# Performance work log

Measured on AMD Instinct MI355X. Metric: run time of the kernel, lower is better.

Reference implementation:

```python
import jax, jax.numpy as jnp
import numpy as np

B, S, DIM, N_CONCEPTS, N_LAYERS = 4, 2048, 1024, 2048, 2


def _phase_linear(x, W, b):
    # x: [b,s,d_in,2]; same real linear applied to real and imag components
    return jnp.einsum('bsdp,od->bsop', x, W) + b[:, None]


def _phase_layernorm(x, gamma, beta, eps=1e-5):
    # per-component LayerNorm over the feature dim with shared affine params
    mu = x.mean(axis=-2, keepdims=True)
    var = x.var(axis=-2, keepdims=True)
    return (x - mu) / jnp.sqrt(var + eps) * gamma[:, None] + beta[:, None]


def setup_inputs() -> dict:
    key = jax.random.key(0)
    ks = jax.random.split(key, 8)
    x = jax.random.normal(ks[0], (B, S, DIM, 2), dtype=jnp.float32)
    concept_memory = jax.random.normal(ks[1], (N_CONCEPTS, DIM, 2), dtype=jnp.float32) * 0.02
    scale = 1.0 / np.sqrt(DIM)
    W_layers = jax.random.normal(ks[2], (N_LAYERS, DIM, DIM), dtype=jnp.float32) * scale
    b_layers = jnp.zeros((N_LAYERS, DIM), dtype=jnp.float32)
    gamma = jnp.ones((N_LAYERS, DIM), dtype=jnp.float32)
    beta = jnp.zeros((N_LAYERS, DIM), dtype=jnp.float32)
    W_out = jax.random.normal(ks[3], (DIM, DIM), dtype=jnp.float32) * scale
    b_out = jnp.zeros((DIM,), dtype=jnp.float32)
    g_out = jnp.ones((DIM,), dtype=jnp.float32)
    beta_out = jnp.zeros((DIM,), dtype=jnp.float32)
    return {"x": x, "concept_memory": concept_memory, "W_layers": W_layers,
            "b_layers": b_layers, "gamma": gamma, "beta": beta,
            "W_out": W_out, "b_out": b_out, "g_out": g_out, "beta_out": beta_out}


def reference(x, concept_memory, W_layers, b_layers, gamma, beta, W_out, b_out, g_out, beta_out):
    xr, xi = x[..., 0], x[..., 1]                       # [b,s,d]
    cr, ci = concept_memory[..., 0], concept_memory[..., 1]  # [n,d]
    # phase-coherence concept attention
    dot_real = jnp.einsum('bsd,nd->bsn', xr, cr) + jnp.einsum('bsd,nd->bsn', xi, ci)
    x_mag = jnp.sqrt((xr ** 2 + xi ** 2).sum(axis=-1, keepdims=True) + 1e-8)   # [b,s,1]
    c_mag = jnp.sqrt((cr ** 2 + ci ** 2).sum(axis=-1) + 1e-8)                  # [n]
    coherence = dot_real / (x_mag * c_mag[None, None, :] + 1e-8)
    concept_attn = jax.nn.softmax(coherence * 2.0, axis=-1)
    concept_retrieved = jnp.einsum('bsn,ndp->bsdp', concept_attn, concept_memory)
    h = x + concept_retrieved * 0.1
    # gated FFN blocks (eval mode: dropout off)
    for l in range(N_LAYERS):
        residual = h
        h = _phase_layernorm(h, gamma[l], beta[l])
        h = _phase_linear(h, W_layers[l], b_layers[l])
        h = jax.nn.gelu(h[..., 0:1], approximate=False) * h
        h = residual + h * 0.1
    out = _phase_layernorm(h, g_out, beta_out)
    out = _phase_linear(out, W_out, b_out)
    return out
```

## Files before the change

kernel.cpp:

```cpp
#include <hip/hip_runtime.h>
#include <hip/hip_bf16.h>

#define ROWS 8192
#define K2   2048
#define NCPT 2048
#define DIMD 1024

using short8 = __attribute__((ext_vector_type(8))) short;
using f32x4  = __attribute__((ext_vector_type(4))) float;

__device__ __forceinline__ unsigned short f2b(float f) {
  __hip_bfloat16 h = __float2bfloat16(f);
  return *reinterpret_cast<unsigned short*>(&h);
}
__device__ __forceinline__ float b2f(unsigned short u) {
  unsigned int x = ((unsigned int)u) << 16;
  return __uint_as_float(x);
}

__device__ __forceinline__ void store_bf16x8(unsigned short* dst, const float4& a, const float4& b) {
  union { unsigned short u[8]; uint4 q; } p;
  p.u[0]=f2b(a.x); p.u[1]=f2b(a.y); p.u[2]=f2b(a.z); p.u[3]=f2b(a.w);
  p.u[4]=f2b(b.x); p.u[5]=f2b(b.y); p.u[6]=f2b(b.z); p.u[7]=f2b(b.w);
  *reinterpret_cast<uint4*>(dst) = p.q;
}
__device__ __forceinline__ void store_bf16x4(unsigned short* dst, float a, float b, float c, float d) {
  union { unsigned short u[4]; uint2 q; } p;
  p.u[0]=f2b(a); p.u[1]=f2b(b); p.u[2]=f2b(c); p.u[3]=f2b(d);
  *reinterpret_cast<uint2*>(dst) = p.q;
}

__device__ __forceinline__ void async_lds16(const void* g, void* l) {
  __builtin_amdgcn_global_load_lds((__attribute__((address_space(1))) void*)g,
                                   (__attribute__((address_space(3))) void*)l, 16, 0, 0);
}

__global__ void cast_row_mag(const float* __restrict__ src, unsigned short* __restrict__ dst,
                             float* __restrict__ mag, int ncol) {
  __shared__ float sred[4];
  int row = blockIdx.x, t = threadIdx.x;
  const float* s = src + (size_t)row * ncol;
  unsigned short* d = dst + (size_t)row * ncol;
  float ss = 0.f;
  for (int i = t * 8; i < ncol; i += 2048) {
    float4 a = *(const float4*)(s + i);
    float4 b = *(const float4*)(s + i + 4);
    ss += a.x*a.x + a.y*a.y + a.z*a.z + a.w*a.w;
    ss += b.x*b.x + b.y*b.y + b.z*b.z + b.w*b.w;
    store_bf16x8(d + i, a, b);
  }
  int lane = t & 63, w = t >> 6;
  for (int o = 32; o; o >>= 1) ss += __shfl_down(ss, o);
  if (lane == 0) sred[w] = ss;
  __syncthreads();
  if (t == 0) mag[row] = sqrtf(sred[0] + sred[1] + sred[2] + sred[3] + 1e-8f);
}

__global__ void cast_f2b(const float* __restrict__ src, unsigned short* __restrict__ dst, int n) {
  int stride = gridDim.x * blockDim.x * 8;
  for (int i = (blockIdx.x * blockDim.x + threadIdx.x) * 8; i < n; i += stride) {
    float4 a = *(const float4*)(src + i);
    float4 b = *(const float4*)(src + i + 4);
    store_bf16x8(dst + i, a, b);
  }
}

__global__ void transpose_f2b(const float* __restrict__ src, unsigned short* __restrict__ dst, int n) {
  __shared__ float tile[32][33];
  int bx = blockIdx.x * 32;
  int by = blockIdx.y * 32;
  int tx = threadIdx.x & 31, ty = threadIdx.x >> 5;
  #pragma unroll
  for (int i = ty; i < 32; i += 8)
    tile[i][tx] = src[(size_t)(by + i) * n + bx + tx];
  __syncthreads();
  #pragma unroll
  for (int i = ty; i < 32; i += 8)
    dst[(size_t)(bx + i) * n + by + tx] = f2b(tile[tx][i]);
}

__global__ void softmax_attn(const unsigned short* __restrict__ logit, unsigned short* __restrict__ attn) {
  __shared__ float sred[4];
  int row = blockIdx.x, t = threadIdx.x;
  int lane = t & 63, w = t >> 6;
  const unsigned short* lr = logit + (size_t)row * NCPT + t * 8;
  short8 lv = *reinterpret_cast<const short8*>(lr);
  float l[8];
  #pragma unroll
  for (int i = 0; i < 8; ++i) l[i] = b2f((unsigned short)lv[i]);
  float m = l[0];
  #pragma unroll
  for (int i = 1; i < 8; ++i) m = fmaxf(m, l[i]);
  for (int o = 32; o; o >>= 1) m = fmaxf(m, __shfl_down(m, o));
  if (lane == 0) sred[w] = m;
  __syncthreads();
  m = fmaxf(fmaxf(sred[0], sred[1]), fmaxf(sred[2], sred[3]));
  __syncthreads();
  float e[8], s = 0.f;
  #pragma unroll
  for (int i = 0; i < 8; ++i) { e[i] = expf(l[i] - m); s += e[i]; }
  for (int o = 32; o; o >>= 1) s += __shfl_down(s, o);
  if (lane == 0) sred[w] = s;
  __syncthreads();
  s = sred[0] + sred[1] + sred[2] + sred[3];
  float inv = 1.f / s;
  float4 A = make_float4(e[0]*inv, e[1]*inv, e[2]*inv, e[3]*inv);
  float4 B = make_float4(e[4]*inv, e[5]*inv, e[6]*inv, e[7]*inv);
  store_bf16x8(attn + (size_t)row * NCPT + t * 8, A, B);
}

__global__ void phase_ln(const float* __restrict__ h, const float* __restrict__ gamma,
                         const float* __restrict__ beta, unsigned short* __restrict__ out) {
  __shared__ float4 s4[4];
  int bs = blockIdx.x, t = threadIdx.x;
  const float* hr = h + (size_t)bs * 2048;
  float4 v0 = *(const float4*)(hr + t * 8);
  float4 v1 = *(const float4*)(hr + t * 8 + 4);
  float r0 = v0.x, i0 = v0.y, r1 = v0.z, i1 = v0.w;
  float r2 = v1.x, i2 = v1.y, r3 = v1.z, i3 = v1.w;
  float4 s;
  s.x = r0 + r1 + r2 + r3;
  s.y = r0*r0 + r1*r1 + r2*r2 + r3*r3;
  s.z = i0 + i1 + i2 + i3;
  s.w = i0*i0 + i1*i1 + i2*i2 + i3*i3;
  int lane = t & 63, w = t >> 6;
  for (int o = 32; o; o >>= 1) {
    s.x += __shfl_down(s.x, o); s.y += __shfl_down(s.y, o);
    s.z += __shfl_down(s.z, o); s.w += __shfl_down(s.w, o);
  }
  if (lane == 0) s4[w] = s;
  __syncthreads();
  float4 T = s4[0];
  #pragma unroll
  for (int i = 1; i < 4; ++i) { T.x += s4[i].x; T.y += s4[i].y; T.z += s4[i].z; T.w += s4[i].w; }
  const float invd = 1.f / 1024.f;
  float mu_r = T.x * invd, var_r = T.y * invd - mu_r * mu_r;
  float mu_i = T.z * invd, var_i = T.w * invd - mu_i * mu_i;
  float is_r = 1.f / sqrtf(var_r + 1e-5f);
  float is_i = 1.f / sqrtf(var_i + 1e-5f);
  float4 g = *(const float4*)(gamma + t * 4);
  float4 b = *(const float4*)(beta + t * 4);
  unsigned short* o0 = out + (size_t)(2 * bs) * 1024 + t * 4;
  unsigned short* o1 = out + (size_t)(2 * bs + 1) * 1024 + t * 4;
  store_bf16x4(o0, (r0-mu_r)*is_r*g.x + b.x, (r1-mu_r)*is_r*g.y + b.y,
                   (r2-mu_r)*is_r*g.z + b.z, (r3-mu_r)*is_r*g.w + b.w);
  store_bf16x4(o1, (i0-mu_i)*is_i*g.x + b.x, (i1-mu_i)*is_i*g.y + b.y,
                   (i2-mu_i)*is_i*g.z + b.z, (i3-mu_i)*is_i*g.w + b.w);
}

template <int EPI>
__global__ __launch_bounds__(512, 2) void gemm256(
    const unsigned short* __restrict__ A, const unsigned short* __restrict__ B,
    int M, int N, int K, void* __restrict__ Cv, const float* __restrict__ aux,
    const float* __restrict__ aux2) {
  __shared__ char lds[131072];
  const int t = threadIdx.x;
  const int l = t & 63;
  const int wid = t >> 6;
  const int wm = wid >> 2, wn = wid & 3;
  const int row0 = blockIdx.y * 256, col0 = blockIdx.x * 256;
  const int NT = K >> 6;

  const int l15 = l & 15, l7 = l & 7, lk = l >> 4;

  f32x4 acc[8][4] = {};
  short8 af[4][2], bf[4][2];

  auto stage = [&](const unsigned short* gmat, int tileRow, int kcol, char* region) {
    const int rsub = t >> 3;
    const int csw = ((t & 7) ^ (rsub & 7)) << 3;
    const unsigned short* g0 = gmat + (size_t)(tileRow + rsub) * K + kcol + csw;
    async_lds16(g0, region + (t & ~63) * 16);
    async_lds16(g0 + (size_t)64 * K, region + 8192 + (t & ~63) * 16);
  };

  stage(A, row0,       0, lds + 0);
  stage(A, row0 + 128, 0, lds + 16384);
  stage(B, col0,       0, lds + 32768);
  stage(B, col0 + 128, 0, lds + 49152);
  if (NT > 1) {
    stage(A, row0, 64, lds + 65536 + 0);
    stage(B, col0, 64, lds + 65536 + 32768);
    asm volatile("s_waitcnt vmcnt(4)" ::: "memory");
  } else {
    asm volatile("s_waitcnt vmcnt(0)" ::: "memory");
  }
  __builtin_amdgcn_s_barrier();
  asm volatile("" ::: "memory");

  for (int tk = 0; tk < NT; ++tk) {
    char* bufC = lds + (tk & 1) * 65536;
    char* bufN = lds + ((tk & 1) ^ 1) * 65536;

    #pragma unroll
    for (int m = 0; m < 4; ++m)
      #pragma unroll
      for (int kh = 0; kh < 2; ++kh) {
        const int r = wm * 64 + m * 16 + l15;
        const int sp = ((((kh << 2) | lk) ^ l7) << 4);
        af[m][kh] = *reinterpret_cast<const short8*>(bufC + r * 128 + sp);
      }
    #pragma unroll
    for (int n = 0; n < 2; ++n)
      #pragma unroll
      for (int kh = 0; kh < 2; ++kh) {
        const int r = wn * 32 + n * 16 + l15;
        const int sp = ((((kh << 2) | lk) ^ l7) << 4);
        bf[n][kh] = *reinterpret_cast<const short8*>(bufC + 32768 + r * 128 + sp);
      }
    if (tk + 1 < NT) stage(A, row0 + 128, (tk + 1) * 64, bufN + 16384);
    asm volatile("" ::: "memory");
    __builtin_amdgcn_s_barrier();
    asm volatile("" ::: "memory");
    __builtin_amdgcn_s_setprio(1);
    #pragma unroll
    for (int kh = 0; kh < 2; ++kh)
      #pragma unroll
      for (int m = 0; m < 4; ++m)
        #pragma unroll
        for (int n = 0; n < 2; ++n)
          acc[m][n] = __builtin_amdgcn_mfma_f32_16x16x32_bf16(af[m][kh], bf[n][kh], acc[m][n], 0, 0, 0);
    __builtin_amdgcn_s_setprio(0);
    asm volatile("" ::: "memory");
    __builtin_amdgcn_s_barrier();
    asm volatile("" ::: "memory");

    #pragma unroll
    for (int n = 2; n < 4; ++n)
      #pragma unroll
      for (int kh = 0; kh < 2; ++kh) {
        const int r = wn * 32 + (n & 1) * 16 + l15;
        const int sp = ((((kh << 2) | lk) ^ l7) << 4);
        bf[n][kh] = *reinterpret_cast<const short8*>(bufC + 49152 + r * 128 + sp);
      }
    if (tk + 1 < NT) stage(B, col0 + 128, (tk + 1) * 64, bufN + 49152);
    asm volatile("" ::: "memory");
    __builtin_amdgcn_s_barrier();
    asm volatile("" ::: "memory");
    __builtin_amdgcn_s_setprio(1);
    #pragma unroll
    for (int kh = 0; kh < 2; ++kh)
      #pragma unroll
      for (int m = 0; m < 4; ++m)
        #pragma unroll
        for (int n = 2; n < 4; ++n)
          acc[m][n] = __builtin_amdgcn_mfma_f32_16x16x32_bf16(af[m][kh], bf[n][kh], acc[m][n], 0, 0, 0);
    __builtin_amdgcn_s_setprio(0);
    asm volatile("" ::: "memory");
    __builtin_amdgcn_s_barrier();
    asm volatile("" ::: "memory");

    #pragma unroll
    for (int m = 0; m < 4; ++m)
      #pragma unroll
      for (int kh = 0; kh < 2; ++kh) {
        const int r = wm * 64 + m * 16 + l15;
        const int sp = ((((kh << 2) | lk) ^ l7) << 4);
        af[m][kh] = *reinterpret_cast<const short8*>(bufC + 16384 + r * 128 + sp);
      }
    if (tk + 2 < NT) stage(A, row0, (tk + 2) * 64, bufC + 0);
    asm volatile("" ::: "memory");
    __builtin_amdgcn_s_barrier();
    asm volatile("" ::: "memory");
    __builtin_amdgcn_s_setprio(1);
    #pragma unroll
    for (int kh = 0; kh < 2; ++kh)
      #pragma unroll
      for (int m = 0; m < 4; ++m)
        #pragma unroll
        for (int n = 0; n < 2; ++n)
          acc[m + 4][n] = __builtin_amdgcn_mfma_f32_16x16x32_bf16(af[m][kh], bf[n][kh], acc[m + 4][n], 0, 0, 0);
    __builtin_amdgcn_s_setprio(0);
    asm volatile("" ::: "memory");
    __builtin_amdgcn_s_barrier();
    asm volatile("" ::: "memory");

    if (tk + 2 < NT) {
      stage(B, col0, (tk + 2) * 64, bufC + 32768);
      asm volatile("s_waitcnt vmcnt(4)" ::: "memory");
    } else {
      asm volatile("s_waitcnt vmcnt(0)" ::: "memory");
    }
    __builtin_amdgcn_s_barrier();
    asm volatile("" ::: "memory");
    __builtin_amdgcn_s_setprio(1);
    #pragma unroll
    for (int kh = 0; kh < 2; ++kh)
      #pragma unroll
      for (int m = 0; m < 4; ++m)
        #pragma unroll
        for (int n = 2; n < 4; ++n)
          acc[m + 4][n] = __builtin_amdgcn_mfma_f32_16x16x32_bf16(af[m][kh], bf[n][kh], acc[m + 4][n], 0, 0, 0);
    __builtin_amdgcn_s_setprio(0);
    asm volatile("" ::: "memory");
    __builtin_amdgcn_s_barrier();
    asm volatile("" ::: "memory");
  }
  asm volatile("s_waitcnt vmcnt(0)" ::: "memory");

  const int cr = lk * 4;
  #pragma unroll
  for (int m = 0; m < 8; ++m) {
    const int gr = row0 + ((m >> 2) << 7) + wm * 64 + ((m & 3) << 4) + cr;
    #pragma unroll
    for (int n = 0; n < 4; ++n) {
      const int gc = col0 + ((n >> 1) << 7) + wn * 32 + ((n & 1) << 4) + l15;
      if constexpr (EPI == 0) {
        unsigned short* C = (unsigned short*)Cv;
        const float cm_ = aux2[gc];
        #pragma unroll
        for (int j = 0; j < 4; ++j) {
          const int r = gr + j;
          float v = 2.f * acc[m][n][j] / (aux[r] * cm_ + 1e-8f);
          C[(size_t)r * N + gc] = f2b(v);
        }
      } else if constexpr (EPI == 1) {
        float* C = (float*)Cv;
        #pragma unroll
        for (int j = 0; j < 4; ++j) {
          const int r = gr + j;
          C[(size_t)r * N + gc] = aux[(size_t)r * N + gc] + 0.1f * acc[m][n][j];
        }
      } else if constexpr (EPI == 2) {
        float* C = (float*)Cv;
        const float bb = aux[gc];
        #pragma unroll
        for (int jj = 0; jj < 2; ++jj) {
          const int r = gr + jj * 2;
          float re = acc[m][n][jj * 2] + bb;
          float im = acc[m][n][jj * 2 + 1] + bb;
          float g = 0.5f * re * (1.f + erff(re * 0.70710678118654752440f));
          size_t idx = (size_t)(r >> 1) * 2048 + (size_t)gc * 2;
          float2 hv = *(float2*)(C + idx);
          hv.x += 0.1f * g * re;
          hv.y += 0.1f * g * im;
          *(float2*)(C + idx) = hv;
        }
      } else {
        float* C = (float*)Cv;
        #pragma unroll
        for (int j = 0; j < 4; ++j) {
          const int r = gr + j;
          C[(size_t)(r >> 1) * 2048 + (size_t)gc * 2 + (r & 1)] = acc[m][n][j] + aux[gc];
        }
      }
    }
  }
}

extern "C" void kernel_launch(void* const* d_in, const int* in_sizes, int n_in,
                              void* d_out, int out_size, void* d_ws, size_t ws_size,
                              hipStream_t stream) {
  const float* x     = (const float*)d_in[0];
  const float* cm    = (const float*)d_in[1];
  const float* Wl    = (const float*)d_in[2];
  const float* bl    = (const float*)d_in[3];
  const float* gamma = (const float*)d_in[4];
  const float* beta  = (const float*)d_in[5];
  const float* Wo    = (const float*)d_in[6];
  const float* bo    = (const float*)d_in[7];
  const float* go    = (const float*)d_in[8];
  const float* bto   = (const float*)d_in[9];
  float* out = (float*)d_out;

  char* p = (char*)d_ws;
  unsigned short* x_bf = (unsigned short*)p; p += (size_t)ROWS * K2 * 2;
  unsigned short* c_bf = (unsigned short*)p; p += (size_t)NCPT * K2 * 2;
  unsigned short* c_T  = (unsigned short*)p; p += (size_t)K2 * NCPT * 2;
  unsigned short* w_bf = (unsigned short*)p; p += (size_t)3 * 1024 * 1024 * 2;
  float* x_mag = (float*)p; p += (size_t)ROWS * 4;
  float* c_mag = (float*)p; p += (size_t)NCPT * 4;
  unsigned short* dot_bf = (unsigned short*)p; p += (size_t)ROWS * NCPT * 2;
  unsigned short* attn   = (unsigned short*)p; p += (size_t)ROWS * NCPT * 2;
  float* h = (float*)p; p += (size_t)ROWS * K2 * 4;
  unsigned short* ln_bf = attn;

  cast_row_mag<<<ROWS, 256, 0, stream>>>(x, x_bf, x_mag, K2);
  cast_row_mag<<<NCPT, 256, 0, stream>>>(cm, c_bf, c_mag, K2);
  transpose_f2b<<<dim3(64, 64), 256, 0, stream>>>(cm, c_T, 2048);
  cast_f2b<<<1024, 256, 0, stream>>>(Wl, w_bf, 2 * 1024 * 1024);
  cast_f2b<<<512, 256, 0, stream>>>(Wo, w_bf + 2 * 1024 * 1024, 1024 * 1024);

  gemm256<0><<<dim3(NCPT / 256, ROWS / 256), 512, 0, stream>>>(
      x_bf, c_bf, ROWS, NCPT, K2, dot_bf, x_mag, c_mag);
  softmax_attn<<<ROWS, 256, 0, stream>>>(dot_bf, attn);
  gemm256<1><<<dim3(K2 / 256, ROWS / 256), 512, 0, stream>>>(
      attn, c_T, ROWS, K2, NCPT, h, x, nullptr);

  for (int l = 0; l < 2; ++l) {
    phase_ln<<<ROWS, 256, 0, stream>>>(h, gamma + l * 1024, beta + l * 1024, ln_bf);
    gemm256<2><<<dim3(DIMD / 256, 2 * ROWS / 256), 512, 0, stream>>>(
        ln_bf, w_bf + (size_t)l * 1024 * 1024, 2 * ROWS, DIMD, DIMD, h, bl + l * 1024, nullptr);
  }

  phase_ln<<<ROWS, 256, 0, stream>>>(h, go, bto, ln_bf);
  gemm256<3><<<dim3(DIMD / 256, 2 * ROWS / 256), 512, 0, stream>>>(
      ln_bf, w_bf + 2 * 1024 * 1024, 2 * ROWS, DIMD, DIMD, out, bo, nullptr);
}
```

Measured before the change: 408.8 us.

## Restructure GEMM prefetch schedule, remap workgroups across XCDs, read residual from bf16

The GEMM pipeline now fully prefetches tile k+1 in the prologue and issues all four quarter-tile loads for k+2 into the current buffer during the loop, waiting on vmcnt(8) and an extra lgkmcnt wait. Workgroup IDs are remapped in chunks of eight so neighbouring tiles land on the same XCD, which should improve L2 reuse. The residual in the attention-output epilogue is read from the bf16 copy of x instead of fp32 x, halving that read traffic but rounding the residual to bf16, which loses precision. A dead readA helper is added. The remap assumes the workgroup count divides by eight, and the prefetch timing changes could introduce races if the waits are wrong.

```diff
diff --git a/kernel.cpp b/kernel.cpp
--- a/kernel.cpp
+++ b/kernel.cpp
@@ -152,15 +152,21 @@
 __global__ __launch_bounds__(512, 2) void gemm256(
     const unsigned short* __restrict__ A, const unsigned short* __restrict__ B,
     int M, int N, int K, void* __restrict__ Cv, const float* __restrict__ aux,
-    const float* __restrict__ aux2) {
+    const float* __restrict__ aux2, const unsigned short* __restrict__ auxb) {
   __shared__ char lds[131072];
   const int t = threadIdx.x;
   const int l = t & 63;
   const int wid = t >> 6;
   const int wm = wid >> 2, wn = wid & 3;
-  const int row0 = blockIdx.y * 256, col0 = blockIdx.x * 256;
+
+  const int nwg = gridDim.x * gridDim.y;
+  int bid = blockIdx.y * gridDim.x + blockIdx.x;
+  const int chunk = nwg >> 3;
+  bid = (bid & 7) * chunk + (bid >> 3);
+  const int row0 = (bid / gridDim.x) * 256;
+  const int col0 = (bid % gridDim.x) * 256;
+
   const int NT = K >> 6;
-
   const int l15 = l & 15, l7 = l & 7, lk = l >> 4;
 
   f32x4 acc[8][4] = {};
@@ -174,14 +180,23 @@
     async_lds16(g0 + (size_t)64 * K, region + 8192 + (t & ~63) * 16);
   };
 
+  auto readA = [&](char* base, int m, int kh) -> short8 {
+    const int r = wm * 64 + m * 16 + l15;
+    const int sp = ((((kh << 1) | (lk >> 1)) * 2 + (lk & 1)) ^ l7) << 4;
+    return *reinterpret_cast<const short8*>(base + r * 128 + sp);
+  };
+  (void)readA;
+
   stage(A, row0,       0, lds + 0);
   stage(A, row0 + 128, 0, lds + 16384);
   stage(B, col0,       0, lds + 32768);
   stage(B, col0 + 128, 0, lds + 49152);
   if (NT > 1) {
-    stage(A, row0, 64, lds + 65536 + 0);
-    stage(B, col0, 64, lds + 65536 + 32768);
-    asm volatile("s_waitcnt vmcnt(4)" ::: "memory");
+    stage(A, row0,       64, lds + 65536 + 0);
+    stage(A, row0 + 128, 64, lds + 65536 + 16384);
+    stage(B, col0,       64, lds + 65536 + 32768);
+    stage(B, col0 + 128, 64, lds + 65536 + 49152);
+    asm volatile("s_waitcnt vmcnt(8)" ::: "memory");
   } else {
     asm volatile("s_waitcnt vmcnt(0)" ::: "memory");
   }
@@ -190,7 +205,8 @@
 
   for (int tk = 0; tk < NT; ++tk) {
     char* bufC = lds + (tk & 1) * 65536;
-    char* bufN = lds + ((tk & 1) ^ 1) * 65536;
+    const bool pf = (tk + 2 < NT);
+    const int kpf = (tk + 2) * 64;
 
     #pragma unroll
     for (int m = 0; m < 4; ++m)
@@ -208,8 +224,7 @@
         const int sp = ((((kh << 2) | lk) ^ l7) << 4);
         bf[n][kh] = *reinterpret_cast<const short8*>(bufC + 32768 + r * 128 + sp);
       }
-    if (tk + 1 < NT) stage(A, row0 + 128, (tk + 1) * 64, bufN + 16384);
-    asm volatile("" ::: "memory");
+    asm volatile("s_waitcnt lgkmcnt(8)" ::: "memory");
     __builtin_amdgcn_s_barrier();
     asm volatile("" ::: "memory");
     __builtin_amdgcn_s_setprio(1);
@@ -233,7 +248,10 @@
         const int sp = ((((kh << 2) | lk) ^ l7) << 4);
         bf[n][kh] = *reinterpret_cast<const short8*>(bufC + 49152 + r * 128 + sp);
       }
-    if (tk + 1 < NT) stage(B, col0 + 128, (tk + 1) * 64, bufN + 49152);
+    if (pf) {
+      stage(A, row0,       kpf, bufC + 0);
+      stage(B, col0,       kpf, bufC + 32768);
+    }
     asm volatile("" ::: "memory");
     __builtin_amdgcn_s_barrier();
     asm volatile("" ::: "memory");
@@ -258,7 +276,7 @@
         const int sp = ((((kh << 2) | lk) ^ l7) << 4);
         af[m][kh] = *reinterpret_cast<const short8*>(bufC + 16384 + r * 128 + sp);
       }
-    if (tk + 2 < NT) stage(A, row0, (tk + 2) * 64, bufC + 0);
+    if (pf) stage(B, col0 + 128, kpf, bufC + 49152);
     asm volatile("" ::: "memory");
     __builtin_amdgcn_s_barrier();
     asm volatile("" ::: "memory");
@@ -275,9 +293,9 @@
     __builtin_amdgcn_s_barrier();
     asm volatile("" ::: "memory");
 
-    if (tk + 2 < NT) {
-      stage(B, col0, (tk + 2) * 64, bufC + 32768);
-      asm volatile("s_waitcnt vmcnt(4)" ::: "memory");
+    if (pf) {
+      stage(A, row0 + 128, kpf, bufC + 16384);
+      asm volatile("s_waitcnt vmcnt(8)" ::: "memory");
     } else {
       asm volatile("s_waitcnt vmcnt(0)" ::: "memory");
     }
@@ -319,7 +337,7 @@
         #pragma unroll
         for (int j = 0; j < 4; ++j) {
           const int r = gr + j;
-          C[(size_t)r * N + gc] = aux[(size_t)r * N + gc] + 0.1f * acc[m][n][j];
+          C[(size_t)r * N + gc] = b2f(auxb[(size_t)r * N + gc]) + 0.1f * acc[m][n][j];
         }
       } else if constexpr (EPI == 2) {
         float* C = (float*)Cv;
@@ -382,18 +400,18 @@
   cast_f2b<<<512, 256, 0, stream>>>(Wo, w_bf + 2 * 1024 * 1024, 1024 * 1024);
 
   gemm256<0><<<dim3(NCPT / 256, ROWS / 256), 512, 0, stream>>>(
-      x_bf, c_bf, ROWS, NCPT, K2, dot_bf, x_mag, c_mag);
+      x_bf, c_bf, ROWS, NCPT, K2, dot_bf, x_mag, c_mag, nullptr);
   softmax_attn<<<ROWS, 256, 0, stream>>>(dot_bf, attn);
   gemm256<1><<<dim3(K2 / 256, ROWS / 256), 512, 0, stream>>>(
-      attn, c_T, ROWS, K2, NCPT, h, x, nullptr);
+      attn, c_T, ROWS, K2, NCPT, h, nullptr, nullptr, x_bf);
 
   for (int l = 0; l < 2; ++l) {
     phase_ln<<<ROWS, 256, 0, stream>>>(h, gamma + l * 1024, beta + l * 1024, ln_bf);
     gemm256<2><<<dim3(DIMD / 256, 2 * ROWS / 256), 512, 0, stream>>>(
-        ln_bf, w_bf + (size_t)l * 1024 * 1024, 2 * ROWS, DIMD, DIMD, h, bl + l * 1024, nullptr);
+        ln_bf, w_bf + (size_t)l * 1024 * 1024, 2 * ROWS, DIMD, DIMD, h, bl + l * 1024, nullptr, nullptr);
   }
 
   phase_ln<<<ROWS, 256, 0, stream>>>(h, go, bto, ln_bf);
   gemm256<3><<<dim3(DIMD / 256, 2 * ROWS / 256), 512, 0, stream>>>(
-      ln_bf, w_bf + 2 * 1024 * 1024, 2 * ROWS, DIMD, DIMD, out, bo, nullptr);
-}
+      ln_bf, w_bf + 2 * 1024 * 1024, 2 * ROWS, DIMD, DIMD, out, bo, nullptr, nullptr);
+}
```

Result: faster. 394.5 us (-3.5%).
